# Kernel tuning notes

Measured on AMD Instinct MI355X. Metric: run time of the kernel, lower is better.

The kernel has to match this reference:

```python
import jax, jax.numpy as jnp
import numpy as np

IN_DIM = 128
D_MODEL = 2 * IN_DIM        # 256, Mamba d_model
D_INNER = 2 * D_MODEL       # 512, expand=2
D_STATE = 16
D_CONV = 4
DT_RANK = (D_MODEL + 15) // 16  # 16
B = 4
C = 1024                    # original channel dim -> Mamba sequence length
EPS = 1e-5


def rmsnorm(x, w):
    return x * jax.lax.rsqrt(jnp.mean(x * x, axis=-1, keepdims=True) + EPS) * w


def conv1x1(x, w, b):
    # x: (B, Cin, L); 1x1 conv == channel matmul
    return jnp.einsum('oi,bil->bol', w, x) + b[None, :, None]


def mamba(u, in_w, conv_w, conv_b, xproj_w, dt_w, dt_b, A_log, Dp, out_w):
    # u: (B, L, D_MODEL) -- faithful mamba_ssm Mamba block (defaults)
    di, K = conv_w.shape
    n = A_log.shape[1]
    r = dt_w.shape[1]
    xz = u @ in_w.T                              # (B,L,2*di)
    xx, z = jnp.split(xz, 2, axis=-1)
    # depthwise causal conv over L
    xt = jnp.pad(jnp.transpose(xx, (0, 2, 1)), ((0, 0), (0, 0), (K - 1, 0)))
    xc = jax.lax.conv_general_dilated(xt, conv_w[:, None, :], (1,), 'VALID',
                                      feature_group_count=di)
    xx = jax.nn.silu(jnp.transpose(xc + conv_b[None, :, None], (0, 2, 1)))
    dbl = xx @ xproj_w.T                         # (B,L,r+2n)
    dt, Bm, Cm = dbl[..., :r], dbl[..., r:r + n], dbl[..., r + n:]
    dt = jax.nn.softplus(dt @ dt_w.T + dt_b)     # (B,L,di)
    A = -jnp.exp(A_log)                          # (di,n)
    dA = jnp.exp(dt[..., None] * A)              # (B,L,di,n)
    dBx = (dt * xx)[..., None] * Bm[:, :, None, :]

    def step(h, inps):
        dA_t, dBx_t, C_t = inps
        h = dA_t * h + dBx_t
        return h, jnp.einsum('bdn,bn->bd', h, C_t)

    h0 = jnp.zeros((u.shape[0], di, n), u.dtype)
    _, ys = jax.lax.scan(step, h0, (jnp.moveaxis(dA, 1, 0),
                                    jnp.moveaxis(dBx, 1, 0),
                                    jnp.moveaxis(Cm, 1, 0)))
    y = jnp.moveaxis(ys, 0, 1) + xx * Dp
    return (y * jax.nn.silu(z)) @ out_w.T


def postnorm_mamba(u, params, norm_w):
    return rmsnorm(mamba(u, *params), norm_w) + u


def _forward(x, W_in, b_in, W_wp, b_wp, W_fp, b_fp, W_bp, b_bp, W_out, b_out,
             norm_w_top,
             f_in_w, f_conv_w, f_conv_b, f_xproj_w, f_dt_w, f_dt_b, f_A_log, f_D, f_out_w, f_norm_w,
             bk_in_w, bk_conv_w, bk_conv_b, bk_xproj_w, bk_dt_w, bk_dt_b, bk_A_log, bk_D, bk_out_w, bk_norm_w):
    residual = x                                  # (B, C, L)
    xn = rmsnorm(x, norm_w_top)                   # RMSNorm over L
    xt = jnp.transpose(xn, (0, 2, 1))             # (B, L, C); L acts as conv channels
    ssm_in = conv1x1(xt, W_in, b_in)              # (B, 2L, C)
    # forward branch
    fwd = conv1x1(ssm_in, W_fp, b_fp)
    fwd = jnp.transpose(fwd, (0, 2, 1))           # (B, C, 2L): Mamba seq=C
    fwd = postnorm_mamba(fwd, (f_in_w, f_conv_w, f_conv_b, f_xproj_w, f_dt_w,
                               f_dt_b, f_A_log, f_D, f_out_w), f_norm_w)
    fwd = jnp.transpose(fwd, (0, 2, 1))           # (B, 2L, C)
    # backward branch (flip along C)
    bwd = conv1x1(ssm_in[:, :, ::-1], W_bp, b_bp)
    bwd = jnp.transpose(bwd, (0, 2, 1))
    bwd = postnorm_mamba(bwd, (bk_in_w, bk_conv_w, bk_conv_b, bk_xproj_w, bk_dt_w,
                               bk_dt_b, bk_A_log, bk_D, bk_out_w), bk_norm_w)
    bwd = jnp.transpose(bwd, (0, 2, 1))[:, :, ::-1]
    # swish gate
    w = conv1x1(xt, W_wp, b_wp)
    w = w * jax.nn.sigmoid(w)
    out = conv1x1(w * fwd + w * bwd, W_out, b_out)  # (B, L, C)
    return jnp.transpose(out, (0, 2, 1)) + residual  # (B, C, L)


def setup_inputs():
    key = jax.random.key(0)
    ks = iter(jax.random.split(key, 64))
    rn = lambda shape, s=0.02: jax.random.normal(next(ks), shape, jnp.float32) * s
    inp = {"x": jax.random.normal(next(ks), (B, C, IN_DIM), jnp.float32)}
    inp["W_in"] = rn((2 * IN_DIM, IN_DIM));   inp["b_in"] = rn((2 * IN_DIM,), 0.1)
    inp["W_wp"] = rn((2 * IN_DIM, IN_DIM));   inp["b_wp"] = rn((2 * IN_DIM,), 0.1)
    inp["W_fp"] = rn((2 * IN_DIM, 2 * IN_DIM)); inp["b_fp"] = rn((2 * IN_DIM,), 0.1)
    inp["W_bp"] = rn((2 * IN_DIM, 2 * IN_DIM)); inp["b_bp"] = rn((2 * IN_DIM,), 0.1)
    inp["W_out"] = rn((IN_DIM, 2 * IN_DIM));  inp["b_out"] = rn((IN_DIM,), 0.1)
    inp["norm_w_top"] = jnp.ones((IN_DIM,), jnp.float32)
    A_init = jnp.log(jnp.broadcast_to(jnp.arange(1, D_STATE + 1, dtype=jnp.float32),
                                      (D_INNER, D_STATE)))
    for p in ("f", "bk"):
        inp[p + "_in_w"] = rn((2 * D_INNER, D_MODEL))
        inp[p + "_conv_w"] = rn((D_INNER, D_CONV), 0.2)
        inp[p + "_conv_b"] = rn((D_INNER,), 0.1)
        inp[p + "_xproj_w"] = rn((DT_RANK + 2 * D_STATE, D_INNER))
        inp[p + "_dt_w"] = rn((D_INNER, DT_RANK), 0.1)
        inp[p + "_dt_b"] = rn((D_INNER,), 0.5)
        inp[p + "_A_log"] = A_init
        inp[p + "_D"] = jnp.ones((D_INNER,), jnp.float32)
        inp[p + "_out_w"] = rn((D_MODEL, D_INNER))
        inp[p + "_norm_w"] = jnp.ones((D_MODEL,), jnp.float32)
    return inp


def reference(x, W_in, b_in, W_wp, b_wp, W_fp, b_fp, W_bp, b_bp, W_out, b_out,
              norm_w_top,
              f_in_w, f_conv_w, f_conv_b, f_xproj_w, f_dt_w, f_dt_b, f_A_log, f_D, f_out_w, f_norm_w,
              bk_in_w, bk_conv_w, bk_conv_b, bk_xproj_w, bk_dt_w, bk_dt_b, bk_A_log, bk_D, bk_out_w, bk_norm_w):
    return _forward(x, W_in, b_in, W_wp, b_wp, W_fp, b_fp, W_bp, b_bp, W_out, b_out,
                    norm_w_top,
                    f_in_w, f_conv_w, f_conv_b, f_xproj_w, f_dt_w, f_dt_b, f_A_log, f_D, f_out_w, f_norm_w,
                    bk_in_w, bk_conv_w, bk_conv_b, bk_xproj_w, bk_dt_w, bk_dt_b, bk_A_log, bk_D, bk_out_w, bk_norm_w)
```

## Files before the change

kernel.cpp:

```cpp
#include <hip/hip_runtime.h>
#include <math.h>

#define C_LEN 1024
#define NROW 4096
#define NCHUNK 32
#define CHUNK 32

typedef __attribute__((ext_vector_type(8))) short short8;
typedef __attribute__((ext_vector_type(4))) float f32x4;

__device__ __forceinline__ float siluf(float x) { return x / (1.f + __expf(-x)); }

__device__ __forceinline__ unsigned short f2bf(float f) {
    unsigned u = __builtin_bit_cast(unsigned, f);
    unsigned r = (u + 0x7FFFu + ((u >> 16) & 1u)) >> 16;
    return (unsigned short)r;
}
__device__ __forceinline__ float bf2f(unsigned short v) {
    unsigned u = ((unsigned)v) << 16;
    return __builtin_bit_cast(float, u);
}

struct WTab {
    const float* s[11];
    unsigned short* d[11];
    int n[11];
};
__global__ __launch_bounds__(256) void k_prep(WTab t, const float* __restrict__ x,
                                              const float* __restrict__ nw,
                                              unsigned short* __restrict__ xn_bf) {
    int seg = blockIdx.y;
    if (seg < 11) {
        int n = t.n[seg];
        int i = (blockIdx.x * 256 + threadIdx.x) * 4;
        if (i < n) {
            float4 v = *(const float4*)(t.s[seg] + i);
            unsigned short* o = t.d[seg] + i;
            o[0] = f2bf(v.x); o[1] = f2bf(v.y); o[2] = f2bf(v.z); o[3] = f2bf(v.w);
        }
    } else {
        int wave = threadIdx.x >> 6, lane = threadIdx.x & 63;
        #pragma unroll
        for (int it = 0; it < 4; ++it) {
            int row = blockIdx.x * 16 + it * 4 + wave;
            float2 v = ((const float2*)(x + (size_t)row * 128))[lane];
            float ss = v.x * v.x + v.y * v.y;
            #pragma unroll
            for (int off = 32; off; off >>= 1) ss += __shfl_xor(ss, off, 64);
            float rs = rsqrtf(ss * (1.f / 128.f) + 1e-5f);
            float2 wv = ((const float2*)nw)[lane];
            ushort2 o;
            o.x = f2bf(v.x * rs * wv.x);
            o.y = f2bf(v.y * rs * wv.y);
            ((ushort2*)(xn_bf + (size_t)row * 128))[lane] = o;
        }
    }
}

__global__ __launch_bounds__(256) void k_gemm_bf(const unsigned short* __restrict__ A,
                                                 const unsigned short* __restrict__ W,
                                                 const float* __restrict__ bias,
                                                 unsigned short* __restrict__ Cbf,
                                                 int N, int K) {
    __shared__ __align__(16) unsigned short As[64 * 72];
    __shared__ __align__(16) unsigned short Bs[64 * 72];
    int tid = threadIdx.x;
    int m0 = blockIdx.y * 64, n0 = blockIdx.x * 64;
    int w = tid >> 6, lane = tid & 63;
    int q = lane >> 4, ln = lane & 15;
    int srow = tid >> 2;
    int sseg = (tid & 3) * 16;

    const unsigned short* pa = A + (size_t)(m0 + srow) * K + sseg;
    const unsigned short* pw = W + (size_t)(n0 + srow) * K + sseg;

    f32x4 acc[4];
    #pragma unroll
    for (int j = 0; j < 4; ++j) acc[j] = (f32x4)(0.f);

    for (int k0 = 0; k0 < K; k0 += 64) {
        *(short8*)&As[srow * 72 + sseg]     = *(const short8*)pa;
        *(short8*)&As[srow * 72 + sseg + 8] = *(const short8*)(pa + 8);
        *(short8*)&Bs[srow * 72 + sseg]     = *(const short8*)pw;
        *(short8*)&Bs[srow * 72 + sseg + 8] = *(const short8*)(pw + 8);
        pa += 64; pw += 64;
        __syncthreads();
        short8 af0 = *(const short8*)&As[(w * 16 + ln) * 72 + q * 8];
        short8 af1 = *(const short8*)&As[(w * 16 + ln) * 72 + 32 + q * 8];
        #pragma unroll
        for (int j = 0; j < 4; ++j) {
            short8 bf0 = *(const short8*)&Bs[(j * 16 + ln) * 72 + q * 8];
            short8 bf1 = *(const short8*)&Bs[(j * 16 + ln) * 72 + 32 + q * 8];
            acc[j] = __builtin_amdgcn_mfma_f32_16x16x32_bf16(af0, bf0, acc[j], 0, 0, 0);
            acc[j] = __builtin_amdgcn_mfma_f32_16x16x32_bf16(af1, bf1, acc[j], 0, 0, 0);
        }
        __syncthreads();
    }
    #pragma unroll
    for (int j = 0; j < 4; ++j) {
        int nn = n0 + j * 16 + ln;
        float bsv = bias[nn];
        #pragma unroll
        for (int r = 0; r < 4; ++r) {
            int m = m0 + w * 16 + q * 4 + r;
            Cbf[(size_t)m * N + nn] = f2bf(acc[j][r] + bsv);
        }
    }
}

__global__ __launch_bounds__(256) void k_gemm3(
        const unsigned short* __restrict__ xn, const unsigned short* __restrict__ ssm,
        const unsigned short* __restrict__ Wfp, const unsigned short* __restrict__ Wbp,
        const unsigned short* __restrict__ Wwp,
        const float* __restrict__ bfp, const float* __restrict__ bbp,
        const float* __restrict__ bwp,
        unsigned short* __restrict__ uf, unsigned short* __restrict__ ub,
        unsigned short* __restrict__ wbuf) {
    __shared__ __align__(16) unsigned short As[64 * 72];
    __shared__ __align__(16) unsigned short Bs[64 * 72];
    int z = blockIdx.z;
    const unsigned short* A = (z == 2) ? xn : ssm;
    const unsigned short* W = (z == 0) ? Wfp : (z == 1) ? Wbp : Wwp;
    const float* bias = (z == 0) ? bfp : (z == 1) ? bbp : bwp;
    unsigned short* C = (z == 0) ? uf : (z == 1) ? ub : wbuf;
    int K = (z == 2) ? 128 : 256;
    int tid = threadIdx.x;
    int m0 = blockIdx.y * 64, n0 = blockIdx.x * 64;
    int w = tid >> 6, lane = tid & 63;
    int q = lane >> 4, ln = lane & 15;
    int srow = tid >> 2;
    int sseg = (tid & 3) * 16;

    int mLog = m0 + srow;
    int mPhys = (z == 1) ? (mLog ^ (C_LEN - 1)) : mLog;
    const unsigned short* pa = A + (size_t)mPhys * K + sseg;
    const unsigned short* pw = W + (size_t)(n0 + srow) * K + sseg;

    f32x4 acc[4];
    #pragma unroll
    for (int j = 0; j < 4; ++j) acc[j] = (f32x4)(0.f);

    for (int k0 = 0; k0 < K; k0 += 64) {
        *(short8*)&As[srow * 72 + sseg]     = *(const short8*)pa;
        *(short8*)&As[srow * 72 + sseg + 8] = *(const short8*)(pa + 8);
        *(short8*)&Bs[srow * 72 + sseg]     = *(const short8*)pw;
        *(short8*)&Bs[srow * 72 + sseg + 8] = *(const short8*)(pw + 8);
        pa += 64; pw += 64;
        __syncthreads();
        short8 af0 = *(const short8*)&As[(w * 16 + ln) * 72 + q * 8];
        short8 af1 = *(const short8*)&As[(w * 16 + ln) * 72 + 32 + q * 8];
        #pragma unroll
        for (int j = 0; j < 4; ++j) {
            short8 bf0 = *(const short8*)&Bs[(j * 16 + ln) * 72 + q * 8];
            short8 bf1 = *(const short8*)&Bs[(j * 16 + ln) * 72 + 32 + q * 8];
            acc[j] = __builtin_amdgcn_mfma_f32_16x16x32_bf16(af0, bf0, acc[j], 0, 0, 0);
            acc[j] = __builtin_amdgcn_mfma_f32_16x16x32_bf16(af1, bf1, acc[j], 0, 0, 0);
        }
        __syncthreads();
    }
    #pragma unroll
    for (int j = 0; j < 4; ++j) {
        int nn = n0 + j * 16 + ln;
        float bsv = bias[nn];
        #pragma unroll
        for (int r = 0; r < 4; ++r) {
            int m = m0 + w * 16 + q * 4 + r;
            float v = acc[j][r] + bsv;
            if (z == 2) v = siluf(v);
            C[(size_t)m * 256 + nn] = f2bf(v);
        }
    }
}

__global__ __launch_bounds__(256) void k_gemm2(
        const unsigned short* __restrict__ A0, const unsigned short* __restrict__ A1,
        const unsigned short* __restrict__ W0, const unsigned short* __restrict__ W1,
        float* __restrict__ Cf0, float* __restrict__ Cf1,
        unsigned short* __restrict__ Cb0, unsigned short* __restrict__ Cb1,
        int N, int K) {
    __shared__ __align__(16) unsigned short As[64 * 72];
    __shared__ __align__(16) unsigned short Bs[64 * 72];
    int p = blockIdx.z;
    const unsigned short* A = p ? A1 : A0;
    const unsigned short* W = p ? W1 : W0;
    float* Cf = p ? Cf1 : Cf0;
    unsigned short* Cbf = p ? Cb1 : Cb0;
    int tid = threadIdx.x;
    int m0 = blockIdx.y * 64, n0 = blockIdx.x * 64;
    int w = tid >> 6, lane = tid & 63;
    int q = lane >> 4, ln = lane & 15;
    int srow = tid >> 2;
    int sseg = (tid & 3) * 16;

    const unsigned short* pa = A + (size_t)(m0 + srow) * K + sseg;
    int nIdx = n0 + srow;
    const unsigned short* pw = W + (size_t)nIdx * K + sseg;
    bool nOK = (nIdx < N);

    f32x4 acc[4];
    #pragma unroll
    for (int j = 0; j < 4; ++j) acc[j] = (f32x4)(0.f);

    for (int k0 = 0; k0 < K; k0 += 64) {
        *(short8*)&As[srow * 72 + sseg]     = *(const short8*)pa;
        *(short8*)&As[srow * 72 + sseg + 8] = *(const short8*)(pa + 8);
        short8 b0 = (short8)(0), b1 = (short8)(0);
        if (nOK) { b0 = *(const short8*)pw; b1 = *(const short8*)(pw + 8); }
        *(short8*)&Bs[srow * 72 + sseg] = b0;
        *(short8*)&Bs[srow * 72 + sseg + 8] = b1;
        pa += 64; pw += 64;
        __syncthreads();
        short8 af0 = *(const short8*)&As[(w * 16 + ln) * 72 + q * 8];
        short8 af1 = *(const short8*)&As[(w * 16 + ln) * 72 + 32 + q * 8];
        #pragma unroll
        for (int j = 0; j < 4; ++j) {
            short8 bf0 = *(const short8*)&Bs[(j * 16 + ln) * 72 + q * 8];
            short8 bf1 = *(const short8*)&Bs[(j * 16 + ln) * 72 + 32 + q * 8];
            acc[j] = __builtin_amdgcn_mfma_f32_16x16x32_bf16(af0, bf0, acc[j], 0, 0, 0);
            acc[j] = __builtin_amdgcn_mfma_f32_16x16x32_bf16(af1, bf1, acc[j], 0, 0, 0);
        }
        __syncthreads();
    }
    #pragma unroll
    for (int j = 0; j < 4; ++j) {
        int nn = n0 + j * 16 + ln;
        if (nn < N) {
            #pragma unroll
            for (int r = 0; r < 4; ++r) {
                int m = m0 + w * 16 + q * 4 + r;
                float v = acc[j][r];
                if (Cf)  Cf[(size_t)m * N + nn] = v;
                if (Cbf) Cbf[(size_t)m * N + nn] = f2bf(v);
            }
        }
    }
}

__global__ __launch_bounds__(256) void k_gemm_comb(const unsigned short* __restrict__ wbuf,
                                                   const unsigned short* __restrict__ mof,
                                                   const unsigned short* __restrict__ mob,
                                                   const unsigned short* __restrict__ W,
                                                   const float* __restrict__ bias,
                                                   const float* __restrict__ resid,
                                                   float* __restrict__ Cf,
                                                   int N, int K) {
    __shared__ __align__(16) unsigned short As[64 * 72];
    __shared__ __align__(16) unsigned short Bs[64 * 72];
    int tid = threadIdx.x;
    int m0 = blockIdx.y * 64, n0 = blockIdx.x * 64;
    int w = tid >> 6, lane = tid & 63;
    int q = lane >> 4, ln = lane & 15;
    int srow = tid >> 2;
    int sseg = (tid & 3) * 16;

    int mLog = m0 + srow;
    int mFlip = mLog ^ (C_LEN - 1);
    int nIdx = n0 + srow;
    const unsigned short* pw = W + (size_t)nIdx * K + sseg;
    bool nOK = (nIdx < N);

    f32x4 acc[4];
    #pragma unroll
    for (int j = 0; j < 4; ++j) acc[j] = (f32x4)(0.f);

    for (int k0 = 0; k0 < K; k0 += 64) {
        size_t off  = (size_t)mLog * 256 + k0 + sseg;
        size_t offb = (size_t)mFlip * 256 + k0 + sseg;
        #pragma unroll
        for (int h = 0; h < 2; ++h) {
            short8 aw = *(const short8*)(wbuf + off + h * 8);
            short8 af = *(const short8*)(mof + off + h * 8);
            short8 ab = *(const short8*)(mob + offb + h * 8);
            short8 av;
            #pragma unroll
            for (int j = 0; j < 8; ++j)
                av[j] = (short)f2bf(bf2f((unsigned short)aw[j]) *
                                    (bf2f((unsigned short)af[j]) + bf2f((unsigned short)ab[j])));
            *(short8*)&As[srow * 72 + sseg + h * 8] = av;
        }
        short8 b0 = (short8)(0), b1 = (short8)(0);
        if (nOK) { b0 = *(const short8*)pw; b1 = *(const short8*)(pw + 8); }
        *(short8*)&Bs[srow * 72 + sseg] = b0;
        *(short8*)&Bs[srow * 72 + sseg + 8] = b1;
        pw += 64;
        __syncthreads();
        short8 af0 = *(const short8*)&As[(w * 16 + ln) * 72 + q * 8];
        short8 af1 = *(const short8*)&As[(w * 16 + ln) * 72 + 32 + q * 8];
        #pragma unroll
        for (int j = 0; j < 4; ++j) {
            short8 bf0 = *(const short8*)&Bs[(j * 16 + ln) * 72 + q * 8];
            short8 bf1 = *(const short8*)&Bs[(j * 16 + ln) * 72 + 32 + q * 8];
            acc[j] = __builtin_amdgcn_mfma_f32_16x16x32_bf16(af0, bf0, acc[j], 0, 0, 0);
            acc[j] = __builtin_amdgcn_mfma_f32_16x16x32_bf16(af1, bf1, acc[j], 0, 0, 0);
        }
        __syncthreads();
    }
    #pragma unroll
    for (int j = 0; j < 4; ++j) {
        int nn = n0 + j * 16 + ln;
        if (nn < N) {
            float bsv = bias[nn];
            #pragma unroll
            for (int r = 0; r < 4; ++r) {
                int m = m0 + w * 16 + q * 4 + r;
                Cf[(size_t)m * N + nn] = acc[j][r] + bsv + resid[(size_t)m * N + nn];
            }
        }
    }
}

__global__ __launch_bounds__(256) void k_conv(const unsigned short* __restrict__ xz0,
                                              const unsigned short* __restrict__ xz1,
                                              const float* __restrict__ cw0,
                                              const float* __restrict__ cw1,
                                              const float* __restrict__ cb0,
                                              const float* __restrict__ cb1,
                                              unsigned short* __restrict__ xc0,
                                              unsigned short* __restrict__ xc1) {
    int pz = blockIdx.z;
    const unsigned short* xz = pz ? xz1 : xz0;
    const float* cw = pz ? cw1 : cw0;
    const float* cb = pz ? cb1 : cb0;
    unsigned short* xconv_bf = pz ? xc1 : xc0;
    int d = blockIdx.x * 256 + threadIdx.x;
    int by = blockIdx.y;
    int b = by >> 6, c0 = (by & 63) * 16;
    float4 cwv = *(const float4*)(cw + d * 4);
    float bias = cb[d];
    const unsigned short* base = xz + (size_t)(b * C_LEN) * 1024 + d;
    float w0 = 0.f, w1 = 0.f, w2 = 0.f;
    if (c0) {
        w0 = bf2f(base[(size_t)(c0 - 3) * 1024]);
        w1 = bf2f(base[(size_t)(c0 - 2) * 1024]);
        w2 = bf2f(base[(size_t)(c0 - 1) * 1024]);
    }
    unsigned short* out = xconv_bf + (size_t)(b * C_LEN + c0) * 512 + d;
    #pragma unroll
    for (int i = 0; i < 16; ++i) {
        float cur = bf2f(base[(size_t)(c0 + i) * 1024]);
        float acc = bias;
        acc = fmaf(cwv.x, w0, acc);
        acc = fmaf(cwv.y, w1, acc);
        acc = fmaf(cwv.z, w2, acc);
        acc = fmaf(cwv.w, cur, acc);
        out[(size_t)i * 512] = f2bf(siluf(acc));
        w0 = w1; w1 = w2; w2 = cur;
    }
}

__global__ __launch_bounds__(256) void k_dtproj(const float* __restrict__ dbl0,
                                                const float* __restrict__ dbl1,
                                                const float* __restrict__ dtw0,
                                                const float* __restrict__ dtw1,
                                                const float* __restrict__ dtb0,
                                                const float* __restrict__ dtb1,
                                                float* __restrict__ dt0,
                                                float* __restrict__ dt1) {
    int pz = blockIdx.z;
    const float* dbl = pz ? dbl1 : dbl0;
    const float* dtw = pz ? dtw1 : dtw0;
    const float* dtb = pz ? dtb1 : dtb0;
    float* dt = pz ? dt1 : dt0;
    int d = blockIdx.x * 256 + threadIdx.x;
    int r0 = blockIdx.y * 8;
    float4 w0 = *(const float4*)(dtw + d * 16);
    float4 w1 = *(const float4*)(dtw + d * 16 + 4);
    float4 w2 = *(const float4*)(dtw + d * 16 + 8);
    float4 w3 = *(const float4*)(dtw + d * 16 + 12);
    float bias = dtb[d];
    #pragma unroll
    for (int rr = 0; rr < 8; ++rr) {
        int r = r0 + rr;
        const float* row = dbl + (size_t)r * 48;
        float s = bias;
        s = fmaf(row[0], w0.x, s);  s = fmaf(row[1], w0.y, s);
        s = fmaf(row[2], w0.z, s);  s = fmaf(row[3], w0.w, s);
        s = fmaf(row[4], w1.x, s);  s = fmaf(row[5], w1.y, s);
        s = fmaf(row[6], w1.z, s);  s = fmaf(row[7], w1.w, s);
        s = fmaf(row[8], w2.x, s);  s = fmaf(row[9], w2.y, s);
        s = fmaf(row[10], w2.z, s); s = fmaf(row[11], w2.w, s);
        s = fmaf(row[12], w3.x, s); s = fmaf(row[13], w3.y, s);
        s = fmaf(row[14], w3.z, s); s = fmaf(row[15], w3.w, s);
        float sp = fmaxf(s, 0.f) + log1pf(__expf(-fabsf(s)));
        dt[(size_t)r * 512 + d] = sp;
    }
}

__global__ __launch_bounds__(256) void k_scan1(const float* __restrict__ dt0,
                                               const float* __restrict__ dt1,
                                               const unsigned short* __restrict__ xc0,
                                               const unsigned short* __restrict__ xc1,
                                               const float* __restrict__ dblA,
                                               const float* __restrict__ dblB,
                                               const float* __restrict__ alog0,
                                               const float* __restrict__ alog1,
                                               float* __restrict__ hfin0,
                                               float* __restrict__ hfin1,
                                               float* __restrict__ Pfin0,
                                               float* __restrict__ Pfin1) {
    int z = blockIdx.z;
    int b = z & 3, p = z >> 2;
    const float* dt = p ? dt1 : dt0;
    const unsigned short* xconv_bf = p ? xc1 : xc0;
    const float* dbl = p ? dblB : dblA;
    const float* A_log = p ? alog1 : alog0;
    float* hfin = p ? hfin1 : hfin0;
    float* Pfin = p ? Pfin1 : Pfin0;
    int tid = threadIdx.x;
    int nh = tid & 1, dl = tid >> 1;
    int k = blockIdx.x, dg = blockIdx.y;
    int d = dg * 128 + dl;
    float4 al0 = *(const float4*)&A_log[d * 16 + nh * 8];
    float4 al1 = *(const float4*)&A_log[d * 16 + nh * 8 + 4];
    float Ac[8] = {-__expf(al0.x), -__expf(al0.y), -__expf(al0.z), -__expf(al0.w),
                   -__expf(al1.x), -__expf(al1.y), -__expf(al1.z), -__expf(al1.w)};
    size_t r0 = (size_t)(b * C_LEN + k * CHUNK);
    const float* pdt = dt + r0 * 512 + d;
    const unsigned short* pxv = xconv_bf + r0 * 512 + d;
    const float* pB  = dbl + r0 * 48 + 16 + nh * 8;
    float h[8] = {0.f, 0.f, 0.f, 0.f, 0.f, 0.f, 0.f, 0.f};
    float sdt = 0.f;
    #pragma unroll 8
    for (int c = 0; c < CHUNK; ++c) {
        float dtv = *pdt;
        float xv  = bf2f(*pxv);
        float4 B0 = *(const float4*)pB;
        float4 B1 = *(const float4*)(pB + 4);
        float dx = dtv * xv;
        float Bv[8] = {B0.x, B0.y, B0.z, B0.w, B1.x, B1.y, B1.z, B1.w};
        #pragma unroll
        for (int j = 0; j < 8; ++j)
            h[j] = fmaf(__expf(dtv * Ac[j]), h[j], dx * Bv[j]);
        sdt += dtv;
        pdt += 512; pxv += 512; pB += 48;
    }
    size_t idx = ((size_t)(b * NCHUNK + k) * 512 + d) * 16 + nh * 8;
    *(float4*)&hfin[idx]     = make_float4(h[0], h[1], h[2], h[3]);
    *(float4*)&hfin[idx + 4] = make_float4(h[4], h[5], h[6], h[7]);
    *(float4*)&Pfin[idx]     = make_float4(__expf(Ac[0] * sdt), __expf(Ac[1] * sdt),
                                           __expf(Ac[2] * sdt), __expf(Ac[3] * sdt));
    *(float4*)&Pfin[idx + 4] = make_float4(__expf(Ac[4] * sdt), __expf(Ac[5] * sdt),
                                           __expf(Ac[6] * sdt), __expf(Ac[7] * sdt));
}

__global__ __launch_bounds__(256) void k_scan2(const float* __restrict__ hfin0,
                                               const float* __restrict__ hfin1,
                                               float* __restrict__ Pfin0,
                                               float* __restrict__ Pfin1) {
    int tt = blockIdx.x * 256 + threadIdx.x;
    int p = tt >> 15;
    int t = tt & 32767;
    const float* hfin = p ? hfin1 : hfin0;
    float* Pfin = p ? Pfin1 : Pfin0;
    int b = t >> 13;
    int dn = t & 8191;
    float carry = 0.f;
    #pragma unroll
    for (int k = 0; k < NCHUNK; ++k) {
        size_t idx = (size_t)(b * NCHUNK + k) * 8192 + dn;
        float pv = Pfin[idx];
        float hf = hfin[idx];
        Pfin[idx] = carry;
        carry = fmaf(pv, carry, hf);
    }
}

__global__ __launch_bounds__(256) void k_scan3(const float* __restrict__ dt0,
                                               const float* __restrict__ dt1,
                                               const unsigned short* __restrict__ xc0,
                                               const unsigned short* __restrict__ xc1,
                                               const float* __restrict__ dblA,
                                               const float* __restrict__ dblB,
                                               const unsigned short* __restrict__ xz0,
                                               const unsigned short* __restrict__ xz1,
                                               const float* __restrict__ alog0,
                                               const float* __restrict__ alog1,
                                               const float* __restrict__ Dp0,
                                               const float* __restrict__ Dp1,
                                               const float* __restrict__ carry0,
                                               const float* __restrict__ carry1,
                                               unsigned short* __restrict__ g0,
                                               unsigned short* __restrict__ g1) {
    int z = blockIdx.z;
    int b = z & 3, p = z >> 2;
    const float* dt = p ? dt1 : dt0;
    const unsigned short* xconv_bf = p ? xc1 : xc0;
    const float* dbl = p ? dblB : dblA;
    const unsigned short* xz = p ? xz1 : xz0;
    const float* A_log = p ? alog1 : alog0;
    const float* Dp = p ? Dp1 : Dp0;
    const float* carryArr = p ? carry1 : carry0;
    unsigned short* gated_bf = p ? g1 : g0;
    int tid = threadIdx.x;
    int nh = tid & 1, dl = tid >> 1;
    int k = blockIdx.x, dg = blockIdx.y;
    int d = dg * 128 + dl;
    float4 al0 = *(const float4*)&A_log[d * 16 + nh * 8];
    float4 al1 = *(const float4*)&A_log[d * 16 + nh * 8 + 4];
    float Ac[8] = {-__expf(al0.x), -__expf(al0.y), -__expf(al0.z), -__expf(al0.w),
                   -__expf(al1.x), -__expf(al1.y), -__expf(al1.z), -__expf(al1.w)};
    float Dd = Dp[d];
    size_t idx = ((size_t)(b * NCHUNK + k) * 512 + d) * 16 + nh * 8;
    float4 h0 = *(const float4*)&carryArr[idx];
    float4 h1 = *(const float4*)&carryArr[idx + 4];
    float h[8] = {h0.x, h0.y, h0.z, h0.w, h1.x, h1.y, h1.z, h1.w};
    size_t r0 = (size_t)(b * C_LEN + k * CHUNK);
    const float* pdt = dt + r0 * 512 + d;
    const unsigned short* pxv = xconv_bf + r0 * 512 + d;
    const float* pB  = dbl + r0 * 48 + 16 + nh * 8;
    const float* pC  = dbl + r0 * 48 + 32 + nh * 8;
    const unsigned short* pz = xz + r0 * 1024 + 512 + d;
    unsigned short* pg = gated_bf + r0 * 512 + d;
    #pragma unroll 4
    for (int c = 0; c < CHUNK; ++c) {
        float dtv = *pdt;
        float xv  = bf2f(*pxv);
        float4 B0 = *(const float4*)pB;
        float4 B1 = *(const float4*)(pB + 4);
        float4 C0 = *(const float4*)pC;
        float4 C1 = *(const float4*)(pC + 4);
        float dx = dtv * xv;
        float Bv[8] = {B0.x, B0.y, B0.z, B0.w, B1.x, B1.y, B1.z, B1.w};
        float Cv[8] = {C0.x, C0.y, C0.z, C0.w, C1.x, C1.y, C1.z, C1.w};
        float contrib = 0.f;
        #pragma unroll
        for (int j = 0; j < 8; ++j) {
            h[j] = fmaf(__expf(dtv * Ac[j]), h[j], dx * Bv[j]);
            contrib = fmaf(h[j], Cv[j], contrib);
        }
        contrib += __shfl_xor(contrib, 1, 64);
        if (nh == 0) {
            float y = contrib + xv * Dd;
            float zv = bf2f(*pz);
            *pg = f2bf(y * siluf(zv));
        }
        pdt += 512; pxv += 512; pB += 48; pC += 48; pz += 1024; pg += 512;
    }
}

__global__ __launch_bounds__(256) void k_postnorm(const unsigned short* __restrict__ mo0,
                                                  const unsigned short* __restrict__ mo1,
                                                  const float* __restrict__ w0,
                                                  const float* __restrict__ w1,
                                                  const unsigned short* __restrict__ u0,
                                                  const unsigned short* __restrict__ u1,
                                                  unsigned short* __restrict__ o0,
                                                  unsigned short* __restrict__ o1) {
    __shared__ float red[4];
    int p = blockIdx.y;
    const unsigned short* mo = p ? mo1 : mo0;
    const float* w = p ? w1 : w0;
    const unsigned short* u = p ? u1 : u0;
    unsigned short* out = p ? o1 : o0;
    int r = blockIdx.x, tid = threadIdx.x;
    float v = bf2f(mo[(size_t)r * 256 + tid]);
    float ss = v * v;
    #pragma unroll
    for (int off = 32; off; off >>= 1) ss += __shfl_xor(ss, off, 64);
    if ((tid & 63) == 0) red[tid >> 6] = ss;
    __syncthreads();
    float tot = red[0] + red[1] + red[2] + red[3];
    float rs = rsqrtf(tot * (1.f / 256.f) + 1e-5f);
    out[(size_t)r * 256 + tid] = f2bf(v * rs * w[tid] + bf2f(u[(size_t)r * 256 + tid]));
}

extern "C" void kernel_launch(void* const* d_in, const int* in_sizes, int n_in,
                              void* d_out, int out_size, void* d_ws, size_t ws_size,
                              hipStream_t stream) {
    const float* x          = (const float*)d_in[0];
    const float* W_in       = (const float*)d_in[1];
    const float* b_in       = (const float*)d_in[2];
    const float* W_wp       = (const float*)d_in[3];
    const float* b_wp       = (const float*)d_in[4];
    const float* W_fp       = (const float*)d_in[5];
    const float* b_fp       = (const float*)d_in[6];
    const float* W_bp       = (const float*)d_in[7];
    const float* b_bp       = (const float*)d_in[8];
    const float* W_out      = (const float*)d_in[9];
    const float* b_out      = (const float*)d_in[10];
    const float* norm_w_top = (const float*)d_in[11];
    const float* mamba_p[2][10];
    for (int p = 0; p < 2; ++p)
        for (int i = 0; i < 10; ++i)
            mamba_p[p][i] = (const float*)d_in[12 + p * 10 + i];

    float* ws = (float*)d_ws;
    float* dblP[2]  = {ws + 0,       ws + 196608};
    float* dtbP[2]  = {ws + 393216,  ws + 2490368};
    float* hfinP[2] = {ws + 4587520, ws + 5636096};
    float* PfinP[2] = {ws + 6684672, ws + 7733248};

    unsigned short* us = (unsigned short*)(ws + 8781824);
    unsigned short* xn_bf   = us + 0;
    unsigned short* ssm_bf  = us + 524288;
    unsigned short* uf_bf   = us + 1572864;
    unsigned short* ub_bf   = us + 2621440;
    unsigned short* wbuf_bf = us + 3670016;
    unsigned short* xzP[2]  = {us + 4718592,  us + 8912896};
    unsigned short* xcP[2]  = {us + 13107200, us + 15204352};
    unsigned short* gP[2]   = {us + 17301504, us + 19398656};
    unsigned short* moP[2]  = {us + 21495808, us + 22544384};
    unsigned short* mof_bf  = us + 23592960;
    unsigned short* mob_bf  = us + 24641536;
    unsigned short* wb      = us + 25690112;
    unsigned short* wb_W_in  = wb + 0;
    unsigned short* wb_W_wp  = wb + 32768;
    unsigned short* wb_W_fp  = wb + 65536;
    unsigned short* wb_W_bp  = wb + 131072;
    unsigned short* wb_W_out = wb + 196608;
    unsigned short* wb_in[2]  = {wb + 229376, wb + 647168};
    unsigned short* wb_xp[2]  = {wb + 491520, wb + 909312};
    unsigned short* wb_outw[2]= {wb + 516096, wb + 933888};

    WTab t;
    t.s[0] = W_in;            t.d[0] = wb_W_in;   t.n[0] = 32768;
    t.s[1] = W_wp;            t.d[1] = wb_W_wp;   t.n[1] = 32768;
    t.s[2] = W_fp;            t.d[2] = wb_W_fp;   t.n[2] = 65536;
    t.s[3] = W_bp;            t.d[3] = wb_W_bp;   t.n[3] = 65536;
    t.s[4] = W_out;           t.d[4] = wb_W_out;  t.n[4] = 32768;
    t.s[5] = mamba_p[0][0];   t.d[5] = wb_in[0];  t.n[5] = 262144;
    t.s[6] = mamba_p[0][3];   t.d[6] = wb_xp[0];  t.n[6] = 24576;
    t.s[7] = mamba_p[0][8];   t.d[7] = wb_outw[0];t.n[7] = 131072;
    t.s[8] = mamba_p[1][0];   t.d[8] = wb_in[1];  t.n[8] = 262144;
    t.s[9] = mamba_p[1][3];   t.d[9] = wb_xp[1];  t.n[9] = 24576;
    t.s[10]= mamba_p[1][8];   t.d[10]= wb_outw[1];t.n[10]= 131072;
    k_prep<<<dim3(256, 12), 256, 0, stream>>>(t, x, norm_w_top, xn_bf);

    k_gemm_bf<<<dim3(4, 64), 256, 0, stream>>>(xn_bf, wb_W_in, b_in, ssm_bf, 256, 128);
    k_gemm3<<<dim3(4, 64, 3), 256, 0, stream>>>(xn_bf, ssm_bf, wb_W_fp, wb_W_bp, wb_W_wp,
                                                b_fp, b_bp, b_wp, uf_bf, ub_bf, wbuf_bf);
    k_gemm2<<<dim3(16, 64, 2), 256, 0, stream>>>(uf_bf, ub_bf, wb_in[0], wb_in[1],
                                                 nullptr, nullptr, xzP[0], xzP[1], 1024, 256);
    k_conv<<<dim3(2, 256, 2), 256, 0, stream>>>(xzP[0], xzP[1],
                                                mamba_p[0][1], mamba_p[1][1],
                                                mamba_p[0][2], mamba_p[1][2],
                                                xcP[0], xcP[1]);
    k_gemm2<<<dim3(1, 64, 2), 256, 0, stream>>>(xcP[0], xcP[1], wb_xp[0], wb_xp[1],
                                                dblP[0], dblP[1], nullptr, nullptr, 48, 512);
    k_dtproj<<<dim3(2, 512, 2), 256, 0, stream>>>(dblP[0], dblP[1],
                                                  mamba_p[0][4], mamba_p[1][4],
                                                  mamba_p[0][5], mamba_p[1][5],
                                                  dtbP[0], dtbP[1]);
    k_scan1<<<dim3(NCHUNK, 4, 8), 256, 0, stream>>>(dtbP[0], dtbP[1], xcP[0], xcP[1],
                                                    dblP[0], dblP[1],
                                                    mamba_p[0][6], mamba_p[1][6],
                                                    hfinP[0], hfinP[1], PfinP[0], PfinP[1]);
    k_scan2<<<256, 256, 0, stream>>>(hfinP[0], hfinP[1], PfinP[0], PfinP[1]);
    k_scan3<<<dim3(NCHUNK, 4, 8), 256, 0, stream>>>(dtbP[0], dtbP[1], xcP[0], xcP[1],
                                                    dblP[0], dblP[1], xzP[0], xzP[1],
                                                    mamba_p[0][6], mamba_p[1][6],
                                                    mamba_p[0][7], mamba_p[1][7],
                                                    PfinP[0], PfinP[1], gP[0], gP[1]);
    k_gemm2<<<dim3(4, 64, 2), 256, 0, stream>>>(gP[0], gP[1], wb_outw[0], wb_outw[1],
                                                nullptr, nullptr, moP[0], moP[1], 256, 512);
    k_postnorm<<<dim3(NROW, 2), 256, 0, stream>>>(moP[0], moP[1],
                                                  mamba_p[0][9], mamba_p[1][9],
                                                  uf_bf, ub_bf, mof_bf, mob_bf);
    k_gemm_comb<<<dim3(2, 64), 256, 0, stream>>>(wbuf_bf, mof_bf, mob_bf, wb_W_out, b_out,
                                                 x, (float*)d_out, 128, 256);
}
```

Measured before the change: 261.4 us.

## Use 128-row GEMM tiles, store dt as bf16, fold carry scan into scan3

Adds a 128x64-tile GEMM kernel for the in_proj and out_proj matmuls so each workgroup reuses the weight tile across more rows. The softplus dt buffer is now stored in bf16, halving its traffic in both scan passes at some cost in precision. The separate carry-propagation kernel is removed: each scan3 block replays the prefix of chunk end-states itself, which saves a launch but makes later chunks do redundant serial work.

Result: slower. 275.2 us (+5.3%).

```diff
diff --git a/kernel.cpp b/kernel.cpp
--- a/kernel.cpp
+++ b/kernel.cpp
@@ -172,11 +172,78 @@
     }
 }
 
-__global__ __launch_bounds__(256) void k_gemm2(
+__global__ __launch_bounds__(256) void k_gemm128(
+        const unsigned short* __restrict__ A0, const unsigned short* __restrict__ A1,
+        const unsigned short* __restrict__ W0, const unsigned short* __restrict__ W1,
+        unsigned short* __restrict__ Cb0, unsigned short* __restrict__ Cb1,
+        int N, int K) {
+    __shared__ __align__(16) unsigned short As[128 * 72];
+    __shared__ __align__(16) unsigned short Bs[64 * 72];
+    int p = blockIdx.z;
+    const unsigned short* A = p ? A1 : A0;
+    const unsigned short* W = p ? W1 : W0;
+    unsigned short* Cbf = p ? Cb1 : Cb0;
+    int tid = threadIdx.x;
+    int m0 = blockIdx.y * 128, n0 = blockIdx.x * 64;
+    int w = tid >> 6, lane = tid & 63;
+    int q = lane >> 4, ln = lane & 15;
+
+    int arow0 = tid >> 1;
+    int aseg0 = (tid & 1) * 32;
+    int brow = tid >> 2, bseg = (tid & 3) * 16;
+    const unsigned short* pa = A + (size_t)(m0 + arow0) * K + aseg0;
+    const unsigned short* pw = W + (size_t)(n0 + brow) * K + bseg;
+
+    f32x4 acc[2][4];
+    #pragma unroll
+    for (int i = 0; i < 2; ++i)
+        #pragma unroll
+        for (int j = 0; j < 4; ++j) acc[i][j] = (f32x4)(0.f);
+
+    for (int k0 = 0; k0 < K; k0 += 64) {
+        #pragma unroll
+        for (int h = 0; h < 4; ++h)
+            *(short8*)&As[arow0 * 72 + aseg0 + h * 8] = *(const short8*)(pa + h * 8);
+        *(short8*)&Bs[brow * 72 + bseg]     = *(const short8*)pw;
+        *(short8*)&Bs[brow * 72 + bseg + 8] = *(const short8*)(pw + 8);
+        pa += 64; pw += 64;
+        __syncthreads();
+        short8 a0[2], a1[2];
+        #pragma unroll
+        for (int i = 0; i < 2; ++i) {
+            int row = w * 32 + i * 16 + ln;
+            a0[i] = *(const short8*)&As[row * 72 + q * 8];
+            a1[i] = *(const short8*)&As[row * 72 + 32 + q * 8];
+        }
+        #pragma unroll
+        for (int j = 0; j < 4; ++j) {
+            short8 bf0 = *(const short8*)&Bs[(j * 16 + ln) * 72 + q * 8];
+            short8 bf1 = *(const short8*)&Bs[(j * 16 + ln) * 72 + 32 + q * 8];
+            #pragma unroll
+            for (int i = 0; i < 2; ++i) {
+                acc[i][j] = __builtin_amdgcn_mfma_f32_16x16x32_bf16(a0[i], bf0, acc[i][j], 0, 0, 0);
+                acc[i][j] = __builtin_amdgcn_mfma_f32_16x16x32_bf16(a1[i], bf1, acc[i][j], 0, 0, 0);
+            }
+        }
+        __syncthreads();
+    }
+    #pragma unroll
+    for (int i = 0; i < 2; ++i)
+        #pragma unroll
+        for (int j = 0; j < 4; ++j) {
+            int nn = n0 + j * 16 + ln;
+            #pragma unroll
+            for (int r = 0; r < 4; ++r) {
+                int m = m0 + w * 32 + i * 16 + q * 4 + r;
+                Cbf[(size_t)m * N + nn] = f2bf(acc[i][j][r]);
+            }
+        }
+}
+
+__global__ __launch_bounds__(256) void k_gemm2f(
         const unsigned short* __restrict__ A0, const unsigned short* __restrict__ A1,
         const unsigned short* __restrict__ W0, const unsigned short* __restrict__ W1,
         float* __restrict__ Cf0, float* __restrict__ Cf1,
-        unsigned short* __restrict__ Cb0, unsigned short* __restrict__ Cb1,
         int N, int K) {
     __shared__ __align__(16) unsigned short As[64 * 72];
     __shared__ __align__(16) unsigned short Bs[64 * 72];
@@ -184,7 +251,6 @@
     const unsigned short* A = p ? A1 : A0;
     const unsigned short* W = p ? W1 : W0;
     float* Cf = p ? Cf1 : Cf0;
-    unsigned short* Cbf = p ? Cb1 : Cb0;
     int tid = threadIdx.x;
     int m0 = blockIdx.y * 64, n0 = blockIdx.x * 64;
     int w = tid >> 6, lane = tid & 63;
@@ -228,9 +294,7 @@
             #pragma unroll
             for (int r = 0; r < 4; ++r) {
                 int m = m0 + w * 16 + q * 4 + r;
-                float v = acc[j][r];
-                if (Cf)  Cf[(size_t)m * N + nn] = v;
-                if (Cbf) Cbf[(size_t)m * N + nn] = f2bf(v);
+                Cf[(size_t)m * N + nn] = acc[j][r];
             }
         }
     }
@@ -354,13 +418,13 @@
                                                 const float* __restrict__ dtw1,
                                                 const float* __restrict__ dtb0,
                                                 const float* __restrict__ dtb1,
-                                                float* __restrict__ dt0,
-                                                float* __restrict__ dt1) {
+                                                unsigned short* __restrict__ dt0,
+                                                unsigned short* __restrict__ dt1) {
     int pz = blockIdx.z;
     const float* dbl = pz ? dbl1 : dbl0;
     const float* dtw = pz ? dtw1 : dtw0;
     const float* dtb = pz ? dtb1 : dtb0;
-    float* dt = pz ? dt1 : dt0;
+    unsigned short* dt = pz ? dt1 : dt0;
     int d = blockIdx.x * 256 + threadIdx.x;
     int r0 = blockIdx.y * 8;
     float4 w0 = *(const float4*)(dtw + d * 16);
@@ -382,12 +446,12 @@
         s = fmaf(row[12], w3.x, s); s = fmaf(row[13], w3.y, s);
         s = fmaf(row[14], w3.z, s); s = fmaf(row[15], w3.w, s);
         float sp = fmaxf(s, 0.f) + log1pf(__expf(-fabsf(s)));
-        dt[(size_t)r * 512 + d] = sp;
-    }
-}
-
-__global__ __launch_bounds__(256) void k_scan1(const float* __restrict__ dt0,
-                                               const float* __restrict__ dt1,
+        dt[(size_t)r * 512 + d] = f2bf(sp);
+    }
+}
+
+__global__ __launch_bounds__(256) void k_scan1(const unsigned short* __restrict__ dt0,
+                                               const unsigned short* __restrict__ dt1,
                                                const unsigned short* __restrict__ xc0,
                                                const unsigned short* __restrict__ xc1,
                                                const float* __restrict__ dblA,
@@ -400,7 +464,7 @@
                                                float* __restrict__ Pfin1) {
     int z = blockIdx.z;
     int b = z & 3, p = z >> 2;
-    const float* dt = p ? dt1 : dt0;
+    const unsigned short* dt = p ? dt1 : dt0;
     const unsigned short* xconv_bf = p ? xc1 : xc0;
     const float* dbl = p ? dblB : dblA;
     const float* A_log = p ? alog1 : alog0;
@@ -415,14 +479,14 @@
     float Ac[8] = {-__expf(al0.x), -__expf(al0.y), -__expf(al0.z), -__expf(al0.w),
                    -__expf(al1.x), -__expf(al1.y), -__expf(al1.z), -__expf(al1.w)};
     size_t r0 = (size_t)(b * C_LEN + k * CHUNK);
-    const float* pdt = dt + r0 * 512 + d;
+    const unsigned short* pdt = dt + r0 * 512 + d;
     const unsigned short* pxv = xconv_bf + r0 * 512 + d;
     const float* pB  = dbl + r0 * 48 + 16 + nh * 8;
     float h[8] = {0.f, 0.f, 0.f, 0.f, 0.f, 0.f, 0.f, 0.f};
     float sdt = 0.f;
     #pragma unroll 8
     for (int c = 0; c < CHUNK; ++c) {
-        float dtv = *pdt;
+        float dtv = bf2f(*pdt);
         float xv  = bf2f(*pxv);
         float4 B0 = *(const float4*)pB;
         float4 B1 = *(const float4*)(pB + 4);
@@ -443,30 +507,8 @@
                                            __expf(Ac[6] * sdt), __expf(Ac[7] * sdt));
 }
 
-__global__ __launch_bounds__(256) void k_scan2(const float* __restrict__ hfin0,
-                                               const float* __restrict__ hfin1,
-                                               float* __restrict__ Pfin0,
-                                               float* __restrict__ Pfin1) {
-    int tt = blockIdx.x * 256 + threadIdx.x;
-    int p = tt >> 15;
-    int t = tt & 32767;
-    const float* hfin = p ? hfin1 : hfin0;
-    float* Pfin = p ? Pfin1 : Pfin0;
-    int b = t >> 13;
-    int dn = t & 8191;
-    float carry = 0.f;
-    #pragma unroll
-    for (int k = 0; k < NCHUNK; ++k) {
-        size_t idx = (size_t)(b * NCHUNK + k) * 8192 + dn;
-        float pv = Pfin[idx];
-        float hf = hfin[idx];
-        Pfin[idx] = carry;
-        carry = fmaf(pv, carry, hf);
-    }
-}
-
-__global__ __launch_bounds__(256) void k_scan3(const float* __restrict__ dt0,
-                                               const float* __restrict__ dt1,
+__global__ __launch_bounds__(256) void k_scan3(const unsigned short* __restrict__ dt0,
+                                               const unsigned short* __restrict__ dt1,
                                                const unsigned short* __restrict__ xc0,
                                                const unsigned short* __restrict__ xc1,
                                                const float* __restrict__ dblA,
@@ -477,19 +519,22 @@
                                                const float* __restrict__ alog1,
                                                const float* __restrict__ Dp0,
                                                const float* __restrict__ Dp1,
-                                               const float* __restrict__ carry0,
-                                               const float* __restrict__ carry1,
+                                               const float* __restrict__ hfin0,
+                                               const float* __restrict__ hfin1,
+                                               const float* __restrict__ Pfin0,
+                                               const float* __restrict__ Pfin1,
                                                unsigned short* __restrict__ g0,
                                                unsigned short* __restrict__ g1) {
     int z = blockIdx.z;
     int b = z & 3, p = z >> 2;
-    const float* dt = p ? dt1 : dt0;
+    const unsigned short* dt = p ? dt1 : dt0;
     const unsigned short* xconv_bf = p ? xc1 : xc0;
     const float* dbl = p ? dblB : dblA;
     const unsigned short* xz = p ? xz1 : xz0;
     const float* A_log = p ? alog1 : alog0;
     const float* Dp = p ? Dp1 : Dp0;
-    const float* carryArr = p ? carry1 : carry0;
+    const float* hfin = p ? hfin1 : hfin0;
+    const float* Pfin = p ? Pfin1 : Pfin0;
     unsigned short* gated_bf = p ? g1 : g0;
     int tid = threadIdx.x;
     int nh = tid & 1, dl = tid >> 1;
@@ -500,12 +545,21 @@
     float Ac[8] = {-__expf(al0.x), -__expf(al0.y), -__expf(al0.z), -__expf(al0.w),
                    -__expf(al1.x), -__expf(al1.y), -__expf(al1.z), -__expf(al1.w)};
     float Dd = Dp[d];
-    size_t idx = ((size_t)(b * NCHUNK + k) * 512 + d) * 16 + nh * 8;
-    float4 h0 = *(const float4*)&carryArr[idx];
-    float4 h1 = *(const float4*)&carryArr[idx + 4];
-    float h[8] = {h0.x, h0.y, h0.z, h0.w, h1.x, h1.y, h1.z, h1.w};
+    float h[8] = {0.f, 0.f, 0.f, 0.f, 0.f, 0.f, 0.f, 0.f};
+    size_t cbase = ((size_t)(b * NCHUNK) * 512 + d) * 16 + nh * 8;
+    for (int j = 0; j < k; ++j) {
+        size_t idx = cbase + (size_t)j * 8192;
+        float4 P0 = *(const float4*)&Pfin[idx];
+        float4 P1 = *(const float4*)&Pfin[idx + 4];
+        float4 H0 = *(const float4*)&hfin[idx];
+        float4 H1 = *(const float4*)&hfin[idx + 4];
+        float Pv[8] = {P0.x, P0.y, P0.z, P0.w, P1.x, P1.y, P1.z, P1.w};
+        float Hv[8] = {H0.x, H0.y, H0.z, H0.w, H1.x, H1.y, H1.z, H1.w};
+        #pragma unroll
+        for (int s = 0; s < 8; ++s) h[s] = fmaf(Pv[s], h[s], Hv[s]);
+    }
     size_t r0 = (size_t)(b * C_LEN + k * CHUNK);
-    const float* pdt = dt + r0 * 512 + d;
+    const unsigned short* pdt = dt + r0 * 512 + d;
     const unsigned short* pxv = xconv_bf + r0 * 512 + d;
     const float* pB  = dbl + r0 * 48 + 16 + nh * 8;
     const float* pC  = dbl + r0 * 48 + 32 + nh * 8;
@@ -513,7 +567,7 @@
     unsigned short* pg = gated_bf + r0 * 512 + d;
     #pragma unroll 4
     for (int c = 0; c < CHUNK; ++c) {
-        float dtv = *pdt;
+        float dtv = bf2f(*pdt);
         float xv  = bf2f(*pxv);
         float4 B0 = *(const float4*)pB;
         float4 B1 = *(const float4*)(pB + 4);
@@ -586,9 +640,10 @@
 
     float* ws = (float*)d_ws;
     float* dblP[2]  = {ws + 0,       ws + 196608};
-    float* dtbP[2]  = {ws + 393216,  ws + 2490368};
     float* hfinP[2] = {ws + 4587520, ws + 5636096};
     float* PfinP[2] = {ws + 6684672, ws + 7733248};
+    unsigned short* dtsP[2] = {(unsigned short*)(ws + 393216),
+                               (unsigned short*)(ws + 2490368)};
 
     unsigned short* us = (unsigned short*)(ws + 8781824);
     unsigned short* xn_bf   = us + 0;
@@ -629,30 +684,30 @@
     k_gemm_bf<<<dim3(4, 64), 256, 0, stream>>>(xn_bf, wb_W_in, b_in, ssm_bf, 256, 128);
     k_gemm3<<<dim3(4, 64, 3), 256, 0, stream>>>(xn_bf, ssm_bf, wb_W_fp, wb_W_bp, wb_W_wp,
                                                 b_fp, b_bp, b_wp, uf_bf, ub_bf, wbuf_bf);
-    k_gemm2<<<dim3(16, 64, 2), 256, 0, stream>>>(uf_bf, ub_bf, wb_in[0], wb_in[1],
-                                                 nullptr, nullptr, xzP[0], xzP[1], 1024, 256);
+    k_gemm128<<<dim3(16, 32, 2), 256, 0, stream>>>(uf_bf, ub_bf, wb_in[0], wb_in[1],
+                                                   xzP[0], xzP[1], 1024, 256);
     k_conv<<<dim3(2, 256, 2), 256, 0, stream>>>(xzP[0], xzP[1],
                                                 mamba_p[0][1], mamba_p[1][1],
                                                 mamba_p[0][2], mamba_p[1][2],
                                                 xcP[0], xcP[1]);
-    k_gemm2<<<dim3(1, 64, 2), 256, 0, stream>>>(xcP[0], xcP[1], wb_xp[0], wb_xp[1],
-                                                dblP[0], dblP[1], nullptr, nullptr, 48, 512);
+    k_gemm2f<<<dim3(1, 64, 2), 256, 0, stream>>>(xcP[0], xcP[1], wb_xp[0], wb_xp[1],
+                                                 dblP[0], dblP[1], 48, 512);
     k_dtproj<<<dim3(2, 512, 2), 256, 0, stream>>>(dblP[0], dblP[1],
                                                   mamba_p[0][4], mamba_p[1][4],
                                                   mamba_p[0][5], mamba_p[1][5],
-                                                  dtbP[0], dtbP[1]);
-    k_scan1<<<dim3(NCHUNK, 4, 8), 256, 0, stream>>>(dtbP[0], dtbP[1], xcP[0], xcP[1],
+                                                  dtsP[0], dtsP[1]);
+    k_scan1<<<dim3(NCHUNK, 4, 8), 256, 0, stream>>>(dtsP[0], dtsP[1], xcP[0], xcP[1],
                                                     dblP[0], dblP[1],
                                                     mamba_p[0][6], mamba_p[1][6],
                                                     hfinP[0], hfinP[1], PfinP[0], PfinP[1]);
-    k_scan2<<<256, 256, 0, stream>>>(hfinP[0], hfinP[1], PfinP[0], PfinP[1]);
-    k_scan3<<<dim3(NCHUNK, 4, 8), 256, 0, stream>>>(dtbP[0], dtbP[1], xcP[0], xcP[1],
+    k_scan3<<<dim3(NCHUNK, 4, 8), 256, 0, stream>>>(dtsP[0], dtsP[1], xcP[0], xcP[1],
                                                     dblP[0], dblP[1], xzP[0], xzP[1],
                                                     mamba_p[0][6], mamba_p[1][6],
                                                     mamba_p[0][7], mamba_p[1][7],
-                                                    PfinP[0], PfinP[1], gP[0], gP[1]);
-    k_gemm2<<<dim3(4, 64, 2), 256, 0, stream>>>(gP[0], gP[1], wb_outw[0], wb_outw[1],
-                                                nullptr, nullptr, moP[0], moP[1], 256, 512);
+                                                    hfinP[0], hfinP[1], PfinP[0], PfinP[1],
+                                                    gP[0], gP[1]);
+    k_gemm128<<<dim3(4, 32, 2), 256, 0, stream>>>(gP[0], gP[1], wb_outw[0], wb_outw[1],
+                                                  moP[0], moP[1], 256, 512);
     k_postnorm<<<dim3(NROW, 2), 256, 0, stream>>>(moP[0], moP[1],
                                                   mamba_p[0][9], mamba_p[1][9],
                                                   uf_bf, ub_bf, mof_bf, mob_bf);
```
